# Kernel optimization log

Measured on AMD Instinct MI355X. Metric: run time of the kernel, lower is better.

## Reference

```python
import jax, jax.numpy as jnp
import numpy as np

DIM = 256
HEADS = 8
HEAD_DIM = DIM // HEADS
RRATIO = 2
EPS = 1e-5


def setup_inputs() -> dict:
    key = jax.random.key(0)
    ks = jax.random.split(key, 6)
    b, nx, ny = 8, 56, 56
    n = 1 + nx * ny  # 1 cls token + spatial tokens
    s = 0.02
    return {
        "x": jax.random.normal(ks[0], (b, n, DIM), jnp.float32),
        "Wq": jax.random.normal(ks[1], (DIM, DIM), jnp.float32) * s,
        "Wkv": jax.random.normal(ks[2], (DIM, 2 * DIM), jnp.float32) * s,
        "conv_w": jax.random.normal(ks[3], (DIM, DIM, RRATIO, RRATIO), jnp.float32) * s,
        "Wproj": jax.random.normal(ks[4], (DIM, DIM), jnp.float32) * s,
        "bproj": jax.random.normal(ks[5], (DIM,), jnp.float32) * s,
        "nx": 56,
        "ny": 56,
    }


def reference(x, Wq, Wkv, conv_w, Wproj, bproj, nx, ny):
    b, n, d = x.shape
    h, dh = HEADS, HEAD_DIM
    scale = dh ** (-0.5)

    # queries: [b,h,n,dh]
    q = (x @ Wq).reshape(b, n, h, dh).transpose(0, 2, 1, 3) * scale

    # spatial reduction of KV tokens: conv stride rratio + instance norm
    x_local = x[:, -nx * ny:].transpose(0, 2, 1).reshape(b, d, nx, ny)  # NCHW
    x_local = jax.lax.conv_general_dilated(
        x_local, conv_w, window_strides=(RRATIO, RRATIO), padding="VALID",
        dimension_numbers=("NCHW", "OIHW", "NCHW"))
    mean = x_local.mean(axis=(2, 3), keepdims=True)
    var = x_local.var(axis=(2, 3), keepdims=True)
    x_local = (x_local - mean) * jax.lax.rsqrt(var + EPS)
    x_local = x_local.reshape(b, d, -1).transpose(0, 2, 1)  # [b, m_sr, d]

    xr = jnp.concatenate([x[:, :-nx * ny], x_local], axis=1)  # [b, m, d]
    m = xr.shape[1]

    kv = xr @ Wkv  # [b, m, 2d]
    k = kv[..., :d].reshape(b, m, h, dh).transpose(0, 2, 1, 3)  # [b,h,m,dh]
    v = kv[..., d:].reshape(b, m, h, dh).transpose(0, 2, 1, 3)

    attn = jnp.einsum("bhnd,bhkd->bhnk", q, k)
    attn = jax.nn.softmax(attn, axis=-1)  # max-subtract softmax is stable softmax
    out = jnp.einsum("bhnk,bhkd->bhnd", attn, v)
    out = out.transpose(0, 2, 1, 3).reshape(b, n, d)
    return out @ Wproj + bproj
```

## Files before the change

kernel.cpp:

```cpp
#include <hip/hip_runtime.h>
#include <math.h>

#define B 8
#define N_TOK 3137
#define D 256
#define H 8
#define DH 32
#define NX 56
#define M_SR 784
#define M_TOK 785
#define MP 832
#define QSCALE 0.25503486f
#define EPS 1e-5f

typedef __attribute__((ext_vector_type(8))) short short8;
typedef __attribute__((ext_vector_type(4))) float f32x4;

#if __has_builtin(__builtin_amdgcn_exp2f)
#define EXP2(x) __builtin_amdgcn_exp2f(x)
#else
#define EXP2(x) exp2f(x)
#endif

static __device__ __forceinline__ unsigned short f2bf(float f) {
    unsigned int u = __float_as_uint(f);
    u += 0x7fffu + ((u >> 16) & 1u);
    return (unsigned short)(u >> 16);
}

static __device__ __forceinline__ void gload16(const unsigned short* g, unsigned short* l) {
    __builtin_amdgcn_global_load_lds(
        (const __attribute__((address_space(1))) unsigned int*)g,
        (__attribute__((address_space(3))) unsigned int*)l,
        16, 0, 0);
}

__global__ void prep_kernel(const float* __restrict__ x, const float* __restrict__ Wq,
                            const float* __restrict__ Wkv, const float* __restrict__ cw,
                            const float* __restrict__ Wproj,
                            unsigned short* __restrict__ xb, unsigned short* __restrict__ Wqt,
                            unsigned short* __restrict__ Wkvt, unsigned short* __restrict__ W2t,
                            unsigned short* __restrict__ Wpt,
                            unsigned short* __restrict__ Kbf, unsigned short* __restrict__ Vtb) {
    int bid = blockIdx.x, tid = threadIdx.x;
    if (bid < 6274) {
        int idx = bid * 256 + tid;
        float4 v = ((const float4*)x)[idx];
        ushort4 o; o.x = f2bf(v.x); o.y = f2bf(v.y); o.z = f2bf(v.z); o.w = f2bf(v.w);
        ((ushort4*)xb)[idx] = o;
    } else if (bid < 6530) {
        int idx = (bid - 6274) * 256 + tid;
        int n = idx & 255, k = idx >> 8;
        Wqt[n * 256 + k] = f2bf(Wq[idx]);
    } else if (bid < 7042) {
        int idx = (bid - 6530) * 256 + tid;
        int n = idx & 511, k = idx >> 9;
        Wkvt[(size_t)n * 256 + k] = f2bf(Wkv[idx]);
    } else if (bid < 8066) {
        int idx = (bid - 7042) * 256 + tid;
        int o = idx >> 10, k = idx & 1023;
        int q = k >> 8, i = k & 255;
        W2t[idx] = f2bf(cw[((size_t)o << 10) + (i << 2) + q]);
    } else if (bid < 8322) {
        int idx = (bid - 8066) * 256 + tid;
        int n = idx & 255, k = idx >> 8;
        Wpt[n * 256 + k] = f2bf(Wproj[idx]);
    } else {
        int idx = (bid - 8322) * 256 + tid;
        if (idx < 96256) {
            int d = idx & 31; int rest = idx >> 5;
            int m = M_TOK + rest % 47; int bh = rest / 47;
            Kbf[((size_t)bh * MP + m) * 32 + d] = 0;
        } else if (idx < 192512) {
            int i2 = idx - 96256;
            int j = i2 % 47; int rest = i2 / 47;
            int d = rest & 31; int bh = rest >> 5;
            Vtb[((size_t)bh * 32 + d) * MP + M_TOK + j] = 0;
        }
    }
}

enum EpiMode { EPI_Q, EPI_XR, EPI_KV, EPI_OUT };
enum AMode { A_PLAIN, A_CONV };

template<int KTOT, AMode AM, EpiMode EM>
__global__ __launch_bounds__(256) void mfma_gemm_kernel(
        const unsigned short* __restrict__ A,
        const unsigned short* __restrict__ Bt,
        void* __restrict__ Cout,
        const float* __restrict__ bias,
        int Mrows) {
    __shared__ __align__(16) unsigned short Alds[64 * 128];
    __shared__ __align__(16) unsigned short Blds[64 * 128];
    const int tid = threadIdx.x;
    const int lane = tid & 63, wave = tid >> 6;
    const int l16 = lane & 15, lhi = lane >> 4;
    const int row0 = blockIdx.x * 64;
    const int col0 = blockIdx.y * 64;
    const int wr = (wave >> 1) * 32, wc = (wave & 1) * 32;

    f32x4 acc[2][2];
    #pragma unroll
    for (int mi = 0; mi < 2; mi++)
        #pragma unroll
        for (int ni = 0; ni < 2; ni++)
            acc[mi][ni] = (f32x4){0.f, 0.f, 0.f, 0.f};

    for (int kc = 0; kc < KTOT / 128; kc++) {
        __syncthreads();
        #pragma unroll
        for (int j = 0; j < 4; j++) {
            int sl = j * 256 + tid;
            int r = sl >> 4, p = sl & 15;
            int s = p ^ (r & 7);
            const unsigned short* gp;
            if (AM == A_PLAIN) {
                gp = A + ((size_t)(row0 + r) * KTOT + kc * 128 + s * 8);
            } else {
                int grow = row0 + r;
                int b = grow / 784, pp = grow - b * 784;
                int oy = pp / 28, ox = pp - oy * 28;
                int q = kc >> 1;
                int kh = q >> 1, kw = q & 1;
                int tok = 1 + (2 * oy + kh) * NX + (2 * ox + kw);
                gp = A + ((size_t)(b * N_TOK + tok) * 256 + (kc & 1) * 128 + s * 8);
            }
            gload16(gp, &Alds[r * 128 + p * 8]);
        }
        #pragma unroll
        for (int j = 0; j < 4; j++) {
            int sl = j * 256 + tid;
            int r = sl >> 4, p = sl & 15;
            int s = p ^ (r & 7);
            gload16(Bt + ((size_t)(col0 + r) * KTOT + kc * 128 + s * 8),
                    &Blds[r * 128 + p * 8]);
        }
        __syncthreads();
        #pragma unroll
        for (int ks = 0; ks < 4; ks++) {
            short8 af[2], bfr[2];
            #pragma unroll
            for (int mi = 0; mi < 2; mi++) {
                int r = wr + mi * 16 + l16;
                int s = ks * 4 + lhi;
                af[mi] = *reinterpret_cast<const short8*>(Alds + r * 128 + ((s ^ (r & 7)) * 8));
            }
            #pragma unroll
            for (int ni = 0; ni < 2; ni++) {
                int r = wc + ni * 16 + l16;
                int s = ks * 4 + lhi;
                bfr[ni] = *reinterpret_cast<const short8*>(Blds + r * 128 + ((s ^ (r & 7)) * 8));
            }
            #pragma unroll
            for (int mi = 0; mi < 2; mi++)
                #pragma unroll
                for (int ni = 0; ni < 2; ni++)
                    acc[mi][ni] = __builtin_amdgcn_mfma_f32_16x16x32_bf16(af[mi], bfr[ni], acc[mi][ni], 0, 0, 0);
        }
    }

    #pragma unroll
    for (int mi = 0; mi < 2; mi++) {
        #pragma unroll
        for (int ni = 0; ni < 2; ni++) {
            #pragma unroll
            for (int r = 0; r < 4; r++) {
                int grow = row0 + wr + mi * 16 + lhi * 4 + r;
                int gcol = col0 + wc + ni * 16 + l16;
                float v = acc[mi][ni][r];
                if (EM == EPI_Q) {
                    if (grow < Mrows) {
                        int b = grow / N_TOK, n = grow - b * N_TOK;
                        int h = gcol >> 5, d = gcol & 31;
                        ((unsigned short*)Cout)[(((size_t)(b * 8 + h) * N_TOK + n) * 32) + d] = f2bf(v * QSCALE);
                    }
                } else if (EM == EPI_XR) {
                    int b = grow / 784, p = grow - b * 784;
                    ((float*)Cout)[((size_t)(b * M_TOK) + 1 + p) * 256 + gcol] = v;
                } else if (EM == EPI_KV) {
                    if (grow < Mrows) {
                        int b = grow / M_TOK, m = grow - b * M_TOK;
                        if (gcol < 256) {
                            int h = gcol >> 5, d = gcol & 31;
                            ((unsigned short*)Cout)[((size_t)(b * 8 + h) * MP + m) * 32 + d] = f2bf(v);
                        } else {
                            int c = gcol - 256;
                            int h = c >> 5, d = c & 31;
                            ((unsigned short*)Cout)[(size_t)64 * MP * 32 + ((size_t)(b * 8 + h) * 32 + d) * MP + m] = f2bf(v);
                        }
                    }
                } else {
                    if (grow < Mrows)
                        ((float*)Cout)[(size_t)grow * 256 + gcol] = v + bias[gcol];
                }
            }
        }
    }
}

__global__ void stats_partial_kernel(const float* __restrict__ XR,
                                     float* __restrict__ psum, float* __restrict__ psq) {
    int b = blockIdx.x / 28, pg = blockIdx.x % 28;
    int c = threadIdx.x;
    float s = 0.f, s2 = 0.f;
    for (int pp = 0; pp < 28; pp++) {
        int p = pg * 28 + pp;
        float v = XR[((size_t)b * M_TOK + 1 + p) * D + c];
        s += v; s2 += v * v;
    }
    psum[(size_t)(b * 28 + pg) * D + c] = s;
    psq [(size_t)(b * 28 + pg) * D + c] = s2;
}

__global__ void stats_final_kernel(const float* __restrict__ psum, const float* __restrict__ psq,
                                   float* __restrict__ mean, float* __restrict__ rstd) {
    int b = blockIdx.x, c = threadIdx.x;
    float s = 0.f, s2 = 0.f;
    for (int pg = 0; pg < 28; pg++) {
        s  += psum[(size_t)(b * 28 + pg) * D + c];
        s2 += psq [(size_t)(b * 28 + pg) * D + c];
    }
    float mu = s * (1.f / 784.f);
    float var = s2 * (1.f / 784.f) - mu * mu;
    mean[b * D + c] = mu;
    rstd[b * D + c] = rsqrtf(var + EPS);
}

__global__ void normalize_kernel(const float* __restrict__ mean, const float* __restrict__ rstd,
                                 const float* __restrict__ XRf, unsigned short* __restrict__ XRb,
                                 const unsigned short* __restrict__ xb) {
    int bid = blockIdx.x;
    if (bid < 6272) {
        int idx = bid * 256 + threadIdx.x;
        int c = idx & 255;
        int bp = idx >> 8;
        int b = bp / 784, p = bp - b * 784;
        size_t off = ((size_t)b * M_TOK + 1 + p) * 256 + c;
        XRb[off] = f2bf((XRf[off] - mean[b * 256 + c]) * rstd[b * 256 + c]);
    } else {
        int b = bid - 6272, c = threadIdx.x;
        XRb[(size_t)b * M_TOK * 256 + c] = xb[(size_t)b * N_TOK * 256 + c];
    }
}

__global__ __launch_bounds__(64) void attn_mfma_kernel(
        const unsigned short* __restrict__ Qbf,
        const unsigned short* __restrict__ Kbf,
        const unsigned short* __restrict__ Vt,
        unsigned short* __restrict__ AObf) {
    __shared__ __align__(16) unsigned short Klds[64 * 32];
    __shared__ __align__(16) unsigned short Vlds[32 * 64];
    const int tid = threadIdx.x;
    const int l16 = tid & 15, lhi = tid >> 4;
    const int sid = (blockIdx.x & 7) * 800 + (blockIdx.x >> 3);
    const int chunk = sid % 100;
    const int bh = sid / 100;
    const int b = bh >> 3, h = bh & 7;
    const int q0 = chunk * 32;

    short8 qf[2];
    #pragma unroll
    for (int qi = 0; qi < 2; qi++) {
        qf[qi] = (short8){0, 0, 0, 0, 0, 0, 0, 0};
        int qrow = q0 + qi * 16 + l16;
        if (qrow < N_TOK)
            qf[qi] = *reinterpret_cast<const short8*>(Qbf + ((size_t)bh * N_TOK + qrow) * 32 + lhi * 8);
    }

    f32x4 o0[2], o1[2];
    float lsum[2];
    #pragma unroll
    for (int qi = 0; qi < 2; qi++) {
        o0[qi] = (f32x4){0.f, 0.f, 0.f, 0.f};
        o1[qi] = (f32x4){0.f, 0.f, 0.f, 0.f};
        lsum[qi] = 0.f;
    }

    const int krow = tid >> 2, kcp = tid & 3;
    const int kclog = kcp ^ ((krow >> 1) & 3);
    const unsigned short* kg = Kbf + ((size_t)bh * MP + krow) * 32 + kclog * 8;
    unsigned short* kl = Klds + tid * 8;
    const int vrow = tid >> 3, vc = tid & 7;
    const int vh = vc >> 2, c2 = vc & 3;
    const unsigned short* vg = Vt + ((size_t)bh * 32 + vrow) * MP + vc * 8;
    const int slotA = vh * 4 + 2 * (c2 & 1);
    const int hoff = (c2 >> 1) * 4;
    unsigned short* vl0 = Vlds + vrow * 64 + ((slotA ^ (vrow & 7)) * 8) + hoff;
    unsigned short* vl1 = Vlds + vrow * 64 + (((slotA + 1) ^ (vrow & 7)) * 8) + hoff;

    for (int t0 = 0; t0 < MP; t0 += 64) {
        __syncthreads();
        #pragma unroll
        for (int rep = 0; rep < 4; rep++) {
            uint4 kd = *reinterpret_cast<const uint4*>(kg + (size_t)t0 * 32 + rep * (16 * 32));
            uint4 vd = *reinterpret_cast<const uint4*>(vg + t0 + (size_t)rep * 8 * MP);
            *reinterpret_cast<uint4*>(kl + rep * 512) = kd;
            *reinterpret_cast<uint2*>(vl0 + rep * 512) = make_uint2(vd.x, vd.y);
            *reinterpret_cast<uint2*>(vl1 + rep * 512) = make_uint2(vd.z, vd.w);
        }
        __syncthreads();
        const bool last = (t0 + 64 > M_TOK);
        #pragma unroll
        for (int hh = 0; hh < 2; hh++) {
            int tre = hh * 32 + l16;
            int tro = hh * 32 + 16 + l16;
            short8 kfe = *reinterpret_cast<const short8*>(
                Klds + tre * 32 + ((lhi ^ ((tre >> 1) & 3)) * 8));
            short8 kfo = *reinterpret_cast<const short8*>(
                Klds + tro * 32 + ((lhi ^ ((tro >> 1) & 3)) * 8));
            int rv0 = l16, rv1 = 16 + l16;
            short8 vf0 = *reinterpret_cast<const short8*>(
                Vlds + rv0 * 64 + (((hh * 4 + lhi) ^ (rv0 & 7)) * 8));
            short8 vf1 = *reinterpret_cast<const short8*>(
                Vlds + rv1 * 64 + (((hh * 4 + lhi) ^ (rv1 & 7)) * 8));
            #pragma unroll
            for (int qi = 0; qi < 2; qi++) {
                f32x4 Se = __builtin_amdgcn_mfma_f32_16x16x32_bf16(
                    kfe, qf[qi], (f32x4){0.f, 0.f, 0.f, 0.f}, 0, 0, 0);
                f32x4 So = __builtin_amdgcn_mfma_f32_16x16x32_bf16(
                    kfo, qf[qi], (f32x4){0.f, 0.f, 0.f, 0.f}, 0, 0, 0);
                float ee0 = EXP2(Se[0]), ee1 = EXP2(Se[1]), ee2 = EXP2(Se[2]), ee3 = EXP2(Se[3]);
                float eo0 = EXP2(So[0]), eo1 = EXP2(So[1]), eo2 = EXP2(So[2]), eo3 = EXP2(So[3]);
                if (!last) {
                    lsum[qi] += ((ee0 + ee1) + (ee2 + ee3)) + ((eo0 + eo1) + (eo2 + eo3));
                } else if (hh == 0) {
                    lsum[qi] += (ee0 + ee1) + (ee2 + ee3);
                    if (lhi == 0) lsum[qi] += eo0;
                }
                union { short8 s; unsigned int u[4]; } pf;
                asm("v_cvt_pk_bf16_f32 %0, %1, %2" : "=v"(pf.u[0]) : "v"(ee0), "v"(ee1));
                asm("v_cvt_pk_bf16_f32 %0, %1, %2" : "=v"(pf.u[1]) : "v"(ee2), "v"(ee3));
                asm("v_cvt_pk_bf16_f32 %0, %1, %2" : "=v"(pf.u[2]) : "v"(eo0), "v"(eo1));
                asm("v_cvt_pk_bf16_f32 %0, %1, %2" : "=v"(pf.u[3]) : "v"(eo2), "v"(eo3));
                o0[qi] = __builtin_amdgcn_mfma_f32_16x16x32_bf16(pf.s, vf0, o0[qi], 0, 0, 0);
                o1[qi] = __builtin_amdgcn_mfma_f32_16x16x32_bf16(pf.s, vf1, o1[qi], 0, 0, 0);
            }
        }
    }
    #pragma unroll
    for (int qi = 0; qi < 2; qi++) {
        lsum[qi] += __shfl_xor(lsum[qi], 16);
        lsum[qi] += __shfl_xor(lsum[qi], 32);
    }
    #pragma unroll
    for (int qi = 0; qi < 2; qi++) {
        #pragma unroll
        for (int r = 0; r < 4; r++) {
            int qrw = lhi * 4 + r;
            float inv = 1.f / __shfl(lsum[qi], qrw);
            int row = q0 + qi * 16 + qrw;
            if (row < N_TOK) {
                unsigned short* op = AObf + ((size_t)(b * N_TOK + row)) * 256 + h * 32;
                op[l16]      = f2bf(o0[qi][r] * inv);
                op[16 + l16] = f2bf(o1[qi][r] * inv);
            }
        }
    }
}

extern "C" void kernel_launch(void* const* d_in, const int* in_sizes, int n_in,
                              void* d_out, int out_size, void* d_ws, size_t ws_size,
                              hipStream_t stream) {
    const float* x      = (const float*)d_in[0];
    const float* Wq     = (const float*)d_in[1];
    const float* Wkv    = (const float*)d_in[2];
    const float* conv_w = (const float*)d_in[3];
    const float* Wproj  = (const float*)d_in[4];
    const float* bproj  = (const float*)d_in[5];
    float* out = (float*)d_out;

    unsigned short* us   = (unsigned short*)d_ws;
    unsigned short* xb   = us;
    unsigned short* AObf = us;
    unsigned short* Qbf  = xb + 6424576;
    unsigned short* Kbf  = Qbf + 6424576;
    unsigned short* Vtb  = Kbf + 1703936;
    unsigned short* XRb  = Vtb + 1703936;
    unsigned short* Wqt  = XRb + 1607680;
    unsigned short* Wkvt = Wqt + 65536;
    unsigned short* W2t  = Wkvt + 131072;
    unsigned short* Wpt  = W2t + 262144;
    float* XRf  = (float*)(Wpt + 65536);
    float* psum = XRf + 1607680;
    float* psq  = psum + 57344;
    float* mean = psq + 57344;
    float* rstd = mean + 2048;

    prep_kernel<<<9075, 256, 0, stream>>>(x, Wq, Wkv, conv_w, Wproj,
                                          xb, Wqt, Wkvt, W2t, Wpt, Kbf, Vtb);
    mfma_gemm_kernel<256, A_PLAIN, EPI_Q><<<dim3(393, 4), 256, 0, stream>>>(
        xb, Wqt, Qbf, nullptr, B * N_TOK);
    mfma_gemm_kernel<1024, A_CONV, EPI_XR><<<dim3(98, 4), 256, 0, stream>>>(
        xb, W2t, XRf, nullptr, B * 784);
    stats_partial_kernel<<<B * 28, 256, 0, stream>>>(XRf, psum, psq);
    stats_final_kernel<<<B, 256, 0, stream>>>(psum, psq, mean, rstd);
    normalize_kernel<<<6280, 256, 0, stream>>>(mean, rstd, XRf, XRb, xb);
    mfma_gemm_kernel<256, A_PLAIN, EPI_KV><<<dim3(99, 8), 256, 0, stream>>>(
        XRb, Wkvt, Kbf, nullptr, B * M_TOK);
    attn_mfma_kernel<<<6400, 64, 0, stream>>>(Qbf, Kbf, Vtb, AObf);
    mfma_gemm_kernel<256, A_PLAIN, EPI_OUT><<<dim3(393, 4), 256, 0, stream>>>(
        AObf, Wpt, out, bproj, B * N_TOK);
}
```

Before: 121.9 us.

## Double-buffer K/V tiles in attention kernel with register prefetch

The attention kernel now holds two LDS buffers for K and V. The next tile's global loads are issued into registers before the current tile's MFMA work and written to the other buffer afterwards. The two __syncthreads per tile are replaced by a waitcnt fence, which is enough because the block is a single 64-thread wavefront. This is meant to hide global load latency behind compute, at the cost of more registers and twice the LDS.

```diff
diff --git a/kernel.cpp b/kernel.cpp
--- a/kernel.cpp
+++ b/kernel.cpp
@@ -21,6 +21,11 @@
 #else
 #define EXP2(x) exp2f(x)
 #endif
+
+#define LDS_FENCE() do { \
+    __builtin_amdgcn_sched_barrier(0); \
+    asm volatile("s_waitcnt lgkmcnt(0)" ::: "memory"); \
+    __builtin_amdgcn_sched_barrier(0); } while (0)
 
 static __device__ __forceinline__ unsigned short f2bf(float f) {
     unsigned int u = __float_as_uint(f);
@@ -248,8 +253,8 @@
         const unsigned short* __restrict__ Kbf,
         const unsigned short* __restrict__ Vt,
         unsigned short* __restrict__ AObf) {
-    __shared__ __align__(16) unsigned short Klds[64 * 32];
-    __shared__ __align__(16) unsigned short Vlds[32 * 64];
+    __shared__ __align__(16) unsigned short Klds[2][64 * 32];
+    __shared__ __align__(16) unsigned short Vlds[2][32 * 64];
     const int tid = threadIdx.x;
     const int l16 = tid & 15, lhi = tid >> 4;
     const int sid = (blockIdx.x & 7) * 800 + (blockIdx.x >> 3);
@@ -279,40 +284,56 @@
     const int krow = tid >> 2, kcp = tid & 3;
     const int kclog = kcp ^ ((krow >> 1) & 3);
     const unsigned short* kg = Kbf + ((size_t)bh * MP + krow) * 32 + kclog * 8;
-    unsigned short* kl = Klds + tid * 8;
+    const int kloff = tid * 8;
     const int vrow = tid >> 3, vc = tid & 7;
     const int vh = vc >> 2, c2 = vc & 3;
     const unsigned short* vg = Vt + ((size_t)bh * 32 + vrow) * MP + vc * 8;
     const int slotA = vh * 4 + 2 * (c2 & 1);
     const int hoff = (c2 >> 1) * 4;
-    unsigned short* vl0 = Vlds + vrow * 64 + ((slotA ^ (vrow & 7)) * 8) + hoff;
-    unsigned short* vl1 = Vlds + vrow * 64 + (((slotA + 1) ^ (vrow & 7)) * 8) + hoff;
-
-    for (int t0 = 0; t0 < MP; t0 += 64) {
-        __syncthreads();
-        #pragma unroll
-        for (int rep = 0; rep < 4; rep++) {
-            uint4 kd = *reinterpret_cast<const uint4*>(kg + (size_t)t0 * 32 + rep * (16 * 32));
-            uint4 vd = *reinterpret_cast<const uint4*>(vg + t0 + (size_t)rep * 8 * MP);
-            *reinterpret_cast<uint4*>(kl + rep * 512) = kd;
-            *reinterpret_cast<uint2*>(vl0 + rep * 512) = make_uint2(vd.x, vd.y);
-            *reinterpret_cast<uint2*>(vl1 + rep * 512) = make_uint2(vd.z, vd.w);
-        }
-        __syncthreads();
+    const int v0off = vrow * 64 + ((slotA ^ (vrow & 7)) * 8) + hoff;
+    const int v1off = vrow * 64 + (((slotA + 1) ^ (vrow & 7)) * 8) + hoff;
+
+    #pragma unroll
+    for (int rep = 0; rep < 4; rep++) {
+        uint4 kd = *reinterpret_cast<const uint4*>(kg + rep * (16 * 32));
+        uint4 vd = *reinterpret_cast<const uint4*>(vg + (size_t)rep * 8 * MP);
+        *reinterpret_cast<uint4*>(&Klds[0][kloff + rep * 512]) = kd;
+        *reinterpret_cast<uint2*>(&Vlds[0][v0off + rep * 512]) = make_uint2(vd.x, vd.y);
+        *reinterpret_cast<uint2*>(&Vlds[0][v1off + rep * 512]) = make_uint2(vd.z, vd.w);
+    }
+    LDS_FENCE();
+
+    #pragma unroll
+    for (int ti = 0; ti < MP / 64; ti++) {
+        const int t0 = ti * 64;
+        const int buf = ti & 1;
+        const bool more = (ti + 1 < MP / 64);
+        uint4 kn[4], vn[4];
+        if (more) {
+            #pragma unroll
+            for (int rep = 0; rep < 4; rep++) {
+                kn[rep] = *reinterpret_cast<const uint4*>(
+                    kg + (size_t)(t0 + 64) * 32 + rep * (16 * 32));
+                vn[rep] = *reinterpret_cast<const uint4*>(
+                    vg + (t0 + 64) + (size_t)rep * 8 * MP);
+            }
+        }
+        const unsigned short* Kb = Klds[buf];
+        const unsigned short* Vb = Vlds[buf];
         const bool last = (t0 + 64 > M_TOK);
         #pragma unroll
         for (int hh = 0; hh < 2; hh++) {
             int tre = hh * 32 + l16;
             int tro = hh * 32 + 16 + l16;
             short8 kfe = *reinterpret_cast<const short8*>(
-                Klds + tre * 32 + ((lhi ^ ((tre >> 1) & 3)) * 8));
+                Kb + tre * 32 + ((lhi ^ ((tre >> 1) & 3)) * 8));
             short8 kfo = *reinterpret_cast<const short8*>(
-                Klds + tro * 32 + ((lhi ^ ((tro >> 1) & 3)) * 8));
+                Kb + tro * 32 + ((lhi ^ ((tro >> 1) & 3)) * 8));
             int rv0 = l16, rv1 = 16 + l16;
             short8 vf0 = *reinterpret_cast<const short8*>(
-                Vlds + rv0 * 64 + (((hh * 4 + lhi) ^ (rv0 & 7)) * 8));
+                Vb + rv0 * 64 + (((hh * 4 + lhi) ^ (rv0 & 7)) * 8));
             short8 vf1 = *reinterpret_cast<const short8*>(
-                Vlds + rv1 * 64 + (((hh * 4 + lhi) ^ (rv1 & 7)) * 8));
+                Vb + rv1 * 64 + (((hh * 4 + lhi) ^ (rv1 & 7)) * 8));
             #pragma unroll
             for (int qi = 0; qi < 2; qi++) {
                 f32x4 Se = __builtin_amdgcn_mfma_f32_16x16x32_bf16(
@@ -336,6 +357,15 @@
                 o1[qi] = __builtin_amdgcn_mfma_f32_16x16x32_bf16(pf.s, vf1, o1[qi], 0, 0, 0);
             }
         }
+        if (more) {
+            #pragma unroll
+            for (int rep = 0; rep < 4; rep++) {
+                *reinterpret_cast<uint4*>(&Klds[buf ^ 1][kloff + rep * 512]) = kn[rep];
+                *reinterpret_cast<uint2*>(&Vlds[buf ^ 1][v0off + rep * 512]) = make_uint2(vn[rep].x, vn[rep].y);
+                *reinterpret_cast<uint2*>(&Vlds[buf ^ 1][v1off + rep * 512]) = make_uint2(vn[rep].z, vn[rep].w);
+            }
+            LDS_FENCE();
+        }
     }
     #pragma unroll
     for (int qi = 0; qi < 2; qi++) {
```

Result: no change. 124.2 us (+1.9%).

## Split attention key range across four waves with LDS reduction

Applied to the files above, without the earlier changes.

The attention kernel now uses 256-thread blocks in which each of four waves processes a quarter of the key/value sequence in its own LDS region. The waves then combine partial outputs and row sums through shared memory, and wave 0 writes the normalized result. K/V padding grows from 832 to 1024 so each wave gets four full 64-key tiles, and the prep kernel zero-fills the larger padding. The aim is more waves in flight and shorter per-wave serial loops, which helps hide latency. The cost is extra padded work, a block-level reduction, and more zero-fill traffic.

```diff
diff --git a/kernel.cpp b/kernel.cpp
--- a/kernel.cpp
+++ b/kernel.cpp
@@ -9,7 +9,7 @@
 #define NX 56
 #define M_SR 784
 #define M_TOK 785
-#define MP 832
+#define MP2 1024
 #define QSCALE 0.25503486f
 #define EPS 1e-5f
 
@@ -21,6 +21,11 @@
 #else
 #define EXP2(x) exp2f(x)
 #endif
+
+#define LDS_FENCE() do { \
+    __builtin_amdgcn_sched_barrier(0); \
+    asm volatile("s_waitcnt lgkmcnt(0)" ::: "memory"); \
+    __builtin_amdgcn_sched_barrier(0); } while (0)
 
 static __device__ __forceinline__ unsigned short f2bf(float f) {
     unsigned int u = __float_as_uint(f);
@@ -67,15 +72,15 @@
         Wpt[n * 256 + k] = f2bf(Wproj[idx]);
     } else {
         int idx = (bid - 8322) * 256 + tid;
-        if (idx < 96256) {
+        if (idx < 489472) {
             int d = idx & 31; int rest = idx >> 5;
-            int m = M_TOK + rest % 47; int bh = rest / 47;
-            Kbf[((size_t)bh * MP + m) * 32 + d] = 0;
-        } else if (idx < 192512) {
-            int i2 = idx - 96256;
-            int j = i2 % 47; int rest = i2 / 47;
+            int m = M_TOK + rest % 239; int bh = rest / 239;
+            Kbf[((size_t)bh * MP2 + m) * 32 + d] = 0;
+        } else if (idx < 978944) {
+            int i2 = idx - 489472;
+            int j = i2 % 239; int rest = i2 / 239;
             int d = rest & 31; int bh = rest >> 5;
-            Vtb[((size_t)bh * 32 + d) * MP + M_TOK + j] = 0;
+            Vtb[((size_t)bh * 32 + d) * MP2 + M_TOK + j] = 0;
         }
     }
 }
@@ -182,11 +187,11 @@
                         int b = grow / M_TOK, m = grow - b * M_TOK;
                         if (gcol < 256) {
                             int h = gcol >> 5, d = gcol & 31;
-                            ((unsigned short*)Cout)[((size_t)(b * 8 + h) * MP + m) * 32 + d] = f2bf(v);
+                            ((unsigned short*)Cout)[((size_t)(b * 8 + h) * MP2 + m) * 32 + d] = f2bf(v);
                         } else {
                             int c = gcol - 256;
                             int h = c >> 5, d = c & 31;
-                            ((unsigned short*)Cout)[(size_t)64 * MP * 32 + ((size_t)(b * 8 + h) * 32 + d) * MP + m] = f2bf(v);
+                            ((unsigned short*)Cout)[(size_t)64 * MP2 * 32 + ((size_t)(b * 8 + h) * 32 + d) * MP2 + m] = f2bf(v);
                         }
                     }
                 } else {
@@ -243,18 +248,18 @@
     }
 }
 
-__global__ __launch_bounds__(64) void attn_mfma_kernel(
+__global__ __launch_bounds__(256) void attn_mfma_kernel(
         const unsigned short* __restrict__ Qbf,
         const unsigned short* __restrict__ Kbf,
         const unsigned short* __restrict__ Vt,
         unsigned short* __restrict__ AObf) {
-    __shared__ __align__(16) unsigned short Klds[64 * 32];
-    __shared__ __align__(16) unsigned short Vlds[32 * 64];
+    __shared__ __align__(16) unsigned short SMEM[4][4096];
     const int tid = threadIdx.x;
-    const int l16 = tid & 15, lhi = tid >> 4;
-    const int sid = (blockIdx.x & 7) * 800 + (blockIdx.x >> 3);
-    const int chunk = sid % 100;
-    const int bh = sid / 100;
+    const int lane = tid & 63, wave = tid >> 6;
+    const int l16 = lane & 15, lhi = lane >> 4;
+    const int sid = (blockIdx.x & 7) * 792 + (blockIdx.x >> 3);
+    const int chunk = sid % 99;
+    const int bh = sid / 99;
     const int b = bh >> 3, h = bh & 7;
     const int q0 = chunk * 32;
 
@@ -276,43 +281,47 @@
         lsum[qi] = 0.f;
     }
 
-    const int krow = tid >> 2, kcp = tid & 3;
+    const int krow = lane >> 2, kcp = lane & 3;
     const int kclog = kcp ^ ((krow >> 1) & 3);
-    const unsigned short* kg = Kbf + ((size_t)bh * MP + krow) * 32 + kclog * 8;
-    unsigned short* kl = Klds + tid * 8;
-    const int vrow = tid >> 3, vc = tid & 7;
+    const unsigned short* kg = Kbf + ((size_t)bh * MP2 + krow) * 32 + kclog * 8;
+    unsigned short* Kl = &SMEM[wave][0] + lane * 8;
+    const int vrow = lane >> 3, vc = lane & 7;
     const int vh = vc >> 2, c2 = vc & 3;
-    const unsigned short* vg = Vt + ((size_t)bh * 32 + vrow) * MP + vc * 8;
+    const unsigned short* vg = Vt + ((size_t)bh * 32 + vrow) * MP2 + vc * 8;
     const int slotA = vh * 4 + 2 * (c2 & 1);
     const int hoff = (c2 >> 1) * 4;
-    unsigned short* vl0 = Vlds + vrow * 64 + ((slotA ^ (vrow & 7)) * 8) + hoff;
-    unsigned short* vl1 = Vlds + vrow * 64 + (((slotA + 1) ^ (vrow & 7)) * 8) + hoff;
-
-    for (int t0 = 0; t0 < MP; t0 += 64) {
-        __syncthreads();
+    unsigned short* Vbase = &SMEM[wave][2048];
+    unsigned short* vl0 = Vbase + vrow * 64 + ((slotA ^ (vrow & 7)) * 8) + hoff;
+    unsigned short* vl1 = Vbase + vrow * 64 + (((slotA + 1) ^ (vrow & 7)) * 8) + hoff;
+    const unsigned short* Kb = &SMEM[wave][0];
+    const unsigned short* Vb = Vbase;
+
+    #pragma unroll
+    for (int i = 0; i < 4; i++) {
+        const int t0 = (wave * 4 + i) * 64;
+        __builtin_amdgcn_sched_barrier(0);
         #pragma unroll
         for (int rep = 0; rep < 4; rep++) {
             uint4 kd = *reinterpret_cast<const uint4*>(kg + (size_t)t0 * 32 + rep * (16 * 32));
-            uint4 vd = *reinterpret_cast<const uint4*>(vg + t0 + (size_t)rep * 8 * MP);
-            *reinterpret_cast<uint4*>(kl + rep * 512) = kd;
+            uint4 vd = *reinterpret_cast<const uint4*>(vg + t0 + (size_t)rep * 8 * MP2);
+            *reinterpret_cast<uint4*>(Kl + rep * 512) = kd;
             *reinterpret_cast<uint2*>(vl0 + rep * 512) = make_uint2(vd.x, vd.y);
             *reinterpret_cast<uint2*>(vl1 + rep * 512) = make_uint2(vd.z, vd.w);
         }
-        __syncthreads();
-        const bool last = (t0 + 64 > M_TOK);
+        LDS_FENCE();
         #pragma unroll
         for (int hh = 0; hh < 2; hh++) {
             int tre = hh * 32 + l16;
             int tro = hh * 32 + 16 + l16;
             short8 kfe = *reinterpret_cast<const short8*>(
-                Klds + tre * 32 + ((lhi ^ ((tre >> 1) & 3)) * 8));
+                Kb + tre * 32 + ((lhi ^ ((tre >> 1) & 3)) * 8));
             short8 kfo = *reinterpret_cast<const short8*>(
-                Klds + tro * 32 + ((lhi ^ ((tro >> 1) & 3)) * 8));
+                Kb + tro * 32 + ((lhi ^ ((tro >> 1) & 3)) * 8));
             int rv0 = l16, rv1 = 16 + l16;
             short8 vf0 = *reinterpret_cast<const short8*>(
-                Vlds + rv0 * 64 + (((hh * 4 + lhi) ^ (rv0 & 7)) * 8));
+                Vb + rv0 * 64 + (((hh * 4 + lhi) ^ (rv0 & 7)) * 8));
             short8 vf1 = *reinterpret_cast<const short8*>(
-                Vlds + rv1 * 64 + (((hh * 4 + lhi) ^ (rv1 & 7)) * 8));
+                Vb + rv1 * 64 + (((hh * 4 + lhi) ^ (rv1 & 7)) * 8));
             #pragma unroll
             for (int qi = 0; qi < 2; qi++) {
                 f32x4 Se = __builtin_amdgcn_mfma_f32_16x16x32_bf16(
@@ -321,9 +330,9 @@
                     kfo, qf[qi], (f32x4){0.f, 0.f, 0.f, 0.f}, 0, 0, 0);
                 float ee0 = EXP2(Se[0]), ee1 = EXP2(Se[1]), ee2 = EXP2(Se[2]), ee3 = EXP2(Se[3]);
                 float eo0 = EXP2(So[0]), eo1 = EXP2(So[1]), eo2 = EXP2(So[2]), eo3 = EXP2(So[3]);
-                if (!last) {
+                if (t0 + 64 <= M_TOK) {
                     lsum[qi] += ((ee0 + ee1) + (ee2 + ee3)) + ((eo0 + eo1) + (eo2 + eo3));
-                } else if (hh == 0) {
+                } else if (t0 < M_TOK && hh == 0) {
                     lsum[qi] += (ee0 + ee1) + (ee2 + ee3);
                     if (lhi == 0) lsum[qi] += eo0;
                 }
@@ -337,22 +346,59 @@
             }
         }
     }
+
+    __syncthreads();
+    float* Mf = reinterpret_cast<float*>(&SMEM[0][0]);
+    const int mbase = (wave * 64 + lane) * 18;
     #pragma unroll
     for (int qi = 0; qi < 2; qi++) {
-        lsum[qi] += __shfl_xor(lsum[qi], 16);
-        lsum[qi] += __shfl_xor(lsum[qi], 32);
-    }
-    #pragma unroll
-    for (int qi = 0; qi < 2; qi++) {
         #pragma unroll
         for (int r = 0; r < 4; r++) {
-            int qrw = lhi * 4 + r;
-            float inv = 1.f / __shfl(lsum[qi], qrw);
-            int row = q0 + qi * 16 + qrw;
-            if (row < N_TOK) {
-                unsigned short* op = AObf + ((size_t)(b * N_TOK + row)) * 256 + h * 32;
-                op[l16]      = f2bf(o0[qi][r] * inv);
-                op[16 + l16] = f2bf(o1[qi][r] * inv);
+            Mf[mbase + qi * 4 + r]     = o0[qi][r];
+            Mf[mbase + 8 + qi * 4 + r] = o1[qi][r];
+        }
+        Mf[mbase + 16 + qi] = lsum[qi];
+    }
+    __syncthreads();
+    if (wave == 0) {
+        f32x4 m0[2], m1[2];
+        float ml[2];
+        #pragma unroll
+        for (int qi = 0; qi < 2; qi++) {
+            m0[qi] = (f32x4){0.f, 0.f, 0.f, 0.f};
+            m1[qi] = (f32x4){0.f, 0.f, 0.f, 0.f};
+            ml[qi] = 0.f;
+        }
+        #pragma unroll
+        for (int w = 0; w < 4; w++) {
+            int wb = (w * 64 + lane) * 18;
+            #pragma unroll
+            for (int qi = 0; qi < 2; qi++) {
+                #pragma unroll
+                for (int r = 0; r < 4; r++) {
+                    m0[qi][r] += Mf[wb + qi * 4 + r];
+                    m1[qi][r] += Mf[wb + 8 + qi * 4 + r];
+                }
+                ml[qi] += Mf[wb + 16 + qi];
+            }
+        }
+        #pragma unroll
+        for (int qi = 0; qi < 2; qi++) {
+            ml[qi] += __shfl_xor(ml[qi], 16);
+            ml[qi] += __shfl_xor(ml[qi], 32);
+        }
+        #pragma unroll
+        for (int qi = 0; qi < 2; qi++) {
+            #pragma unroll
+            for (int r = 0; r < 4; r++) {
+                int qrw = lhi * 4 + r;
+                float inv = 1.f / __shfl(ml[qi], qrw);
+                int row = q0 + qi * 16 + qrw;
+                if (row < N_TOK) {
+                    unsigned short* op = AObf + ((size_t)(b * N_TOK + row)) * 256 + h * 32;
+                    op[l16]      = f2bf(m0[qi][r] * inv);
+                    op[16 + l16] = f2bf(m1[qi][r] * inv);
+                }
             }
         }
     }
@@ -374,8 +420,8 @@
     unsigned short* AObf = us;
     unsigned short* Qbf  = xb + 6424576;
     unsigned short* Kbf  = Qbf + 6424576;
-    unsigned short* Vtb  = Kbf + 1703936;
-    unsigned short* XRb  = Vtb + 1703936;
+    unsigned short* Vtb  = Kbf + 2097152;
+    unsigned short* XRb  = Vtb + 2097152;
     unsigned short* Wqt  = XRb + 1607680;
     unsigned short* Wkvt = Wqt + 65536;
     unsigned short* W2t  = Wkvt + 131072;
@@ -386,8 +432,8 @@
     float* mean = psq + 57344;
     float* rstd = mean + 2048;
 
-    prep_kernel<<<9075, 256, 0, stream>>>(x, Wq, Wkv, conv_w, Wproj,
-                                          xb, Wqt, Wkvt, W2t, Wpt, Kbf, Vtb);
+    prep_kernel<<<12146, 256, 0, stream>>>(x, Wq, Wkv, conv_w, Wproj,
+                                           xb, Wqt, Wkvt, W2t, Wpt, Kbf, Vtb);
     mfma_gemm_kernel<256, A_PLAIN, EPI_Q><<<dim3(393, 4), 256, 0, stream>>>(
         xb, Wqt, Qbf, nullptr, B * N_TOK);
     mfma_gemm_kernel<1024, A_CONV, EPI_XR><<<dim3(98, 4), 256, 0, stream>>>(
@@ -397,7 +443,7 @@
     normalize_kernel<<<6280, 256, 0, stream>>>(mean, rstd, XRf, XRb, xb);
     mfma_gemm_kernel<256, A_PLAIN, EPI_KV><<<dim3(99, 8), 256, 0, stream>>>(
         XRb, Wkvt, Kbf, nullptr, B * M_TOK);
-    attn_mfma_kernel<<<6400, 64, 0, stream>>>(Qbf, Kbf, Vtb, AObf);
+    attn_mfma_kernel<<<6336, 256, 0, stream>>>(Qbf, Kbf, Vtb, AObf);
     mfma_gemm_kernel<256, A_PLAIN, EPI_OUT><<<dim3(393, 4), 256, 0, stream>>>(
         AObf, Wpt, out, bproj, B * N_TOK);
 }
```

New measurement: 133.0 us. 9.1% more time.
